# Optimization experiments

Hardware: AMD Instinct MI355X
Metric: run time of the kernel (lower is better)

## Reference

```python
import jax, jax.numpy as jnp
import numpy as np

N = 50000      # nodes
E = 800000     # edges (avg degree 16)
D_IN, D_H, D_OUT = 128, 128, 64


def setup_inputs() -> dict:
    key = jax.random.key(0)
    ks = jax.random.split(key, 12)
    s = 0.05  # weight init scale
    return {
        "x": jax.random.normal(ks[0], (N, D_IN), jnp.float32),
        "edge_index": jax.random.randint(ks[1], (2, E), 0, N, dtype=jnp.int64),
        "Wl0": jax.random.normal(ks[2], (D_H, D_IN), jnp.float32) * s,
        "bl0": jax.random.normal(ks[3], (D_H,), jnp.float32) * s,
        "Wr0": jax.random.normal(ks[4], (D_H, D_IN), jnp.float32) * s,
        "Wl1": jax.random.normal(ks[5], (D_H, D_H), jnp.float32) * s,
        "bl1": jax.random.normal(ks[6], (D_H,), jnp.float32) * s,
        "Wr1": jax.random.normal(ks[7], (D_H, D_H), jnp.float32) * s,
        "Wl2": jax.random.normal(ks[8], (D_OUT, D_H), jnp.float32) * s,
        "bl2": jax.random.normal(ks[9], (D_OUT,), jnp.float32) * s,
        "Wr2": jax.random.normal(ks[10], (D_OUT, D_H), jnp.float32) * s,
    }


def _sage_layer(h, src, dst, Wl, bl, Wr):
    # mean aggregation over incoming neighbors: out[i] = mean_{j in N(i)} h[j]
    n = h.shape[0]
    agg = jax.ops.segment_sum(h[src], dst, num_segments=n)          # [N, D]
    deg = jax.ops.segment_sum(jnp.ones((src.shape[0],), h.dtype), dst,
                              num_segments=n)                        # [N]
    mean = agg / jnp.maximum(deg, 1.0)[:, None]  # empty rows -> 0, matches torch_sparse
    # lin_l(agg) + lin_r(self); lin_r has no bias in PyG SAGEConv
    return mean @ Wl.T + bl + h @ Wr.T


def reference(x, edge_index, Wl0, bl0, Wr0, Wl1, bl1, Wr1, Wl2, bl2, Wr2):
    src, dst = edge_index[1], edge_index[0]  # adj row = dst, col = src
    h = jax.nn.relu(_sage_layer(x, src, dst, Wl0, bl0, Wr0))
    h = jax.nn.relu(_sage_layer(h, src, dst, Wl1, bl1, Wr1))
    h = _sage_layer(h, src, dst, Wl2, bl2, Wr2)
    return jax.nn.log_softmax(h, axis=1)
```

## Files before the change

kernel.cpp:

```cpp
#include <hip/hip_runtime.h>
#include <hip/hip_bf16.h>


typedef __attribute__((ext_vector_type(8))) short bf16x8;
typedef __attribute__((ext_vector_type(4))) float f32x4;

#define NPB 128
#define BCAP 2560
#define EPB 8192
#define EPT 32
#define CPAD 16

__device__ __forceinline__ unsigned short f2bf(float f) {
    unsigned int u = __builtin_bit_cast(unsigned int, f);
    u += 0x7fffu + ((u >> 16) & 1u);
    return (unsigned short)(u >> 16);
}
__device__ __forceinline__ float bf2f(unsigned int bits16) {
    return __builtin_bit_cast(float, bits16 << 16);
}


__global__ __launch_bounds__(256) void dist_cast_kernel(const int* __restrict__ dst,
                                                        const int* __restrict__ srcv,
                                                        int* __restrict__ gcnt,
                                                        unsigned int* __restrict__ staging,
                                                        int E, int NBc, int DB, int XB,
                                                        const float* __restrict__ x,
                                                        unsigned short* __restrict__ xbf,
                                                        const float* p0, const float* p1,
                                                        const float* p2, const float* p3,
                                                        const float* p4, const float* p5,
                                                        unsigned short* __restrict__ wbf) {
    __shared__ unsigned int stage[EPB];
    __shared__ int hist[400];
    __shared__ int lstart[400];
    __shared__ int gbase[400];
    __shared__ int scanbuf[256];
    int bid = blockIdx.x;
    int t = threadIdx.x;

    if (bid >= DB && bid < DB + XB) {
        int base = (bid - DB) * 256 + t;
        int stride = XB * 256;
        const float2* x2 = (const float2*)x;
        unsigned int* xo = (unsigned int*)xbf;
#pragma unroll
        for (int k = 0; k < 4; ++k) {
            int idx = base + k * stride;
            float2 v = x2[idx];
            xo[idx] = (unsigned int)f2bf(v.x) | ((unsigned int)f2bf(v.y) << 16);
        }
        return;
    }
    if (bid >= DB + XB) {
        int w = (bid - DB - XB) * 256 + t;
        if (w < 40960) {
            const float* src;
            int local;
            if      (w < 8192)  { src = p0; local = w; }
            else if (w < 16384) { src = p1; local = w - 8192; }
            else if (w < 24576) { src = p2; local = w - 16384; }
            else if (w < 32768) { src = p3; local = w - 24576; }
            else if (w < 36864) { src = p4; local = w - 32768; }
            else                { src = p5; local = w - 36864; }
            float2 v = ((const float2*)src)[local];
            unsigned int p = (unsigned int)f2bf(v.x) | ((unsigned int)f2bf(v.y) << 16);
            ((unsigned int*)wbf)[w] = p;
        }
        return;
    }

    int e0 = bid * EPB;
    unsigned int w[EPT];

    for (int b = t; b < NBc + 1; b += 256) hist[b] = 0;
    __syncthreads();

#pragma unroll
    for (int i = 0; i < EPT; ++i) {
        int e = e0 + i * 256 + t;
        unsigned int word = 0xFFFFFFFFu;
        if (e < E) word = ((unsigned int)dst[e] << 16) | (unsigned int)srcv[e];
        w[i] = word;
        int b = (int)(word >> 23); if (b > NBc) b = NBc;
        atomicAdd(&hist[b], 1);
    }
    __syncthreads();

    int b0 = 2 * t, b1 = 2 * t + 1;
    int h0 = (b0 <= NBc) ? hist[b0] : 0;
    int h1 = (b1 <= NBc) ? hist[b1] : 0;
    int pair = h0 + h1;
    scanbuf[t] = pair;
    __syncthreads();
    for (int off = 1; off < 256; off <<= 1) {
        int v = (t >= off) ? scanbuf[t - off] : 0;
        __syncthreads();
        scanbuf[t] += v;
        __syncthreads();
    }
    int excl = scanbuf[t] - pair;
    if (b0 <= NBc) lstart[b0] = excl;
    if (b1 <= NBc) lstart[b1] = excl + h0;
    __syncthreads();

    for (int b = t; b < NBc; b += 256) {
        int h = hist[b];
        gbase[b] = h ? atomicAdd(&gcnt[b * CPAD], h) : 0;
    }
    for (int b = t; b < NBc + 1; b += 256) hist[b] = lstart[b];
    __syncthreads();

#pragma unroll
    for (int i = 0; i < EPT; ++i) {
        unsigned int word = w[i];
        int b = (int)(word >> 23); if (b > NBc) b = NBc;
        int p = atomicAdd(&hist[b], 1);
        stage[p] = word;
    }
    __syncthreads();

    int total = lstart[NBc];
    for (int i = t; i < total; i += 256) {
        unsigned int word = stage[i];
        int b = (int)(word >> 23);
        int gpos = gbase[b] + (i - lstart[b]);
        staging[(size_t)b * BCAP + gpos] = word;
    }
}


template<int GY, int ASL, int CSL>
__device__ __forceinline__ void gemm_body(int mb, int y,
                                          const unsigned short* __restrict__ H,
                                          const unsigned short* __restrict__ Wl,
                                          const unsigned short* __restrict__ Wr,
                                          unsigned short* __restrict__ Cl,
                                          unsigned short* __restrict__ Cr, int N) {
    __shared__ unsigned short clds[4 * 32 * 68];
    const int halfY = GY >> 1;
    const int ldc = GY * 32;
    int wave = threadIdx.x >> 6;
    int lane = threadIdx.x & 63;
    int l15 = lane & 15, quad = lane >> 4;
    bool isL = y < halfY;
    const unsigned short* W = isL ? Wl : Wr;
    unsigned short* Cp = isL ? Cl : Cr;
    int yy = isL ? y : y - halfY;
    int wrow0 = yy * 64;
    int col0 = yy * 64;
    int m0 = mb * 128 + wave * 32;

    int r0 = m0 + l15;      if (r0 > N - 1) r0 = N - 1;
    int r1 = m0 + 16 + l15; if (r1 > N - 1) r1 = N - 1;

    f32x4 acc[2][4] = {};
#pragma unroll
    for (int ks = 0; ks < 4; ++ks) {
        int vidx = ks * 4 + quad;
        bf16x8 a0, a1;
        if constexpr (ASL) {
            const unsigned short* base = H + (size_t)(vidx >> 1) * N * 16 + (vidx & 1) * 8;
            a0 = *(const bf16x8*)(base + (size_t)r0 * 16);
            a1 = *(const bf16x8*)(base + (size_t)r1 * 16);
        } else {
            a0 = ((const bf16x8*)(H + (size_t)r0 * 128))[vidx];
            a1 = ((const bf16x8*)(H + (size_t)r1 * 128))[vidx];
        }
#pragma unroll
        for (int j = 0; j < 4; ++j) {
            const bf16x8* B = (const bf16x8*)(W + (size_t)(wrow0 + j * 16 + l15) * 128);
            bf16x8 b = B[vidx];
            acc[0][j] = __builtin_amdgcn_mfma_f32_16x16x32_bf16(a0, b, acc[0][j], 0, 0, 0);
            acc[1][j] = __builtin_amdgcn_mfma_f32_16x16x32_bf16(a1, b, acc[1][j], 0, 0, 0);
        }
    }

    unsigned short* slice = clds + wave * (32 * 68);
#pragma unroll
    for (int i = 0; i < 2; ++i)
#pragma unroll
        for (int j = 0; j < 4; ++j)
#pragma unroll
            for (int r = 0; r < 4; ++r)
                slice[(i * 16 + quad * 4 + r) * 68 + j * 16 + l15] = f2bf(acc[i][j][r]);
    __syncthreads();

    if (CSL && isL) {
        int nodeLocal = lane >> 1, hf = lane & 1;
        int row = m0 + nodeLocal;
        int s0 = col0 >> 4;
        if (row < N) {
#pragma unroll
            for (int sl = 0; sl < 4; ++sl) {
                const unsigned short* p = slice + nodeLocal * 68 + sl * 16 + hf * 8;
                unsigned long long lo = *(const unsigned long long*)(p);
                unsigned long long hi = *(const unsigned long long*)(p + 4);
                unsigned long long* q =
                    (unsigned long long*)(Cl + ((size_t)(s0 + sl) * N + row) * 16 + hf * 8);
                q[0] = lo;
                q[1] = hi;
            }
        }
    } else {
        int rlo = lane >> 3, j8 = lane & 7;
#pragma unroll
        for (int pass = 0; pass < 4; ++pass) {
            int row_local = pass * 8 + rlo;
            const unsigned short* p = slice + row_local * 68 + j8 * 8;
            unsigned long long lo = *(const unsigned long long*)(p);
            unsigned long long hi = *(const unsigned long long*)(p + 4);
            int row = m0 + row_local;
            if (row < N) {
                unsigned long long* q =
                    (unsigned long long*)(Cp + (size_t)row * ldc + col0 + j8 * 8);
                q[0] = lo;
                q[1] = hi;
            }
        }
    }
    __syncthreads();
}


__global__ __launch_bounds__(256) void build_gemm_kernel(const unsigned int* __restrict__ staging,
                                                         const int* __restrict__ gcnt,
                                                         int* __restrict__ row_ptr,
                                                         int* __restrict__ adj, int N, int NBc,
                                                         int gemmRows,
                                                         const unsigned short* __restrict__ H,
                                                         const unsigned short* __restrict__ Wl,
                                                         const unsigned short* __restrict__ Wr,
                                                         unsigned short* __restrict__ Cl,
                                                         unsigned short* __restrict__ Cr) {
    __shared__ int hist[NPB];
    __shared__ int scn[NPB];
    __shared__ int wsum[4];
    int bid = blockIdx.x;
    int t = threadIdx.x;

    if (bid >= NBc) {
        int gid = bid - NBc;
        gemm_body<4, 0, 1>(gid % gemmRows, gid / gemmRows, H, Wl, Wr, Cl, Cr, N);
        return;
    }

    int b = bid;
    int n0 = b * NPB;
    int nb = N - n0; if (nb > NPB) nb = NPB;
    int ec = gcnt[b * CPAD];
    const unsigned int* st = staging + (size_t)b * BCAP;

    int a = 0;
    for (int j = t; j < b; j += 256) a += gcnt[j * CPAD];
#pragma unroll
    for (int off = 32; off; off >>= 1) a += __shfl_xor(a, off);
    if ((t & 63) == 0) wsum[t >> 6] = a;
    if (t < NPB) hist[t] = 0;
    __syncthreads();
    int bb = wsum[0] + wsum[1] + wsum[2] + wsum[3];

    for (int i = t; i < ec; i += 256)
        atomicAdd(&hist[(st[i] >> 16) & (NPB - 1)], 1);
    __syncthreads();

    int v = (t < NPB) ? hist[t] : 0;
    if (t < NPB) scn[t] = v;
    __syncthreads();
    for (int off = 1; off < NPB; off <<= 1) {
        int u = (t >= off && t < NPB) ? scn[t - off] : 0;
        __syncthreads();
        if (t < NPB) scn[t] += u;
        __syncthreads();
    }
    if (t < NPB) hist[t] = scn[t] - v;
    if (t < nb) row_ptr[n0 + t] = bb + (scn[t] - v);
    if (b == NBc - 1 && t == 0) row_ptr[N] = bb + ec;
    __syncthreads();

    for (int i = t; i < ec; i += 256) {
        unsigned int pk = st[i];
        int p = atomicAdd(&hist[(pk >> 16) & (NPB - 1)], 1);
        adj[bb + p] = (int)(pk & 0xffffu);
    }
}


template<int GY, int ASL, int CSL>
__global__ __launch_bounds__(256) void gemm_mfma_kernel(const unsigned short* __restrict__ H,
                                                        const unsigned short* __restrict__ Wl,
                                                        const unsigned short* __restrict__ Wr,
                                                        unsigned short* __restrict__ Cl,
                                                        unsigned short* __restrict__ Cr,
                                                        int N) {
    gemm_body<GY, ASL, CSL>(blockIdx.x, blockIdx.y, H, Wl, Wr, Cl, Cr, N);
}


__global__ __launch_bounds__(256) void agg_sliced_kernel(const unsigned short* __restrict__ Cls,
                                                         const unsigned short* __restrict__ Cr,
                                                         const int* __restrict__ row_ptr,
                                                         const int* __restrict__ adj,
                                                         const float* __restrict__ bias,
                                                         unsigned short* __restrict__ houts,
                                                         int N) {
    int s = blockIdx.x & 7;
    int nb = blockIdx.x >> 3;
    int wave = threadIdx.x >> 6;
    int lane = threadIdx.x & 63;
    int node = nb * 128 + wave * 32 + (lane >> 1);
    int half = lane & 1;
    if (node >= N) return;
    int beg = row_ptr[node], end = row_ptr[node + 1];
    const unsigned short* tab = Cls + (size_t)s * N * 16 + half * 8;

    float acc[8] = {};
    int e = beg;
    for (; e + 4 <= end; e += 4) {
        int i0 = adj[e], i1 = adj[e + 1], i2 = adj[e + 2], i3 = adj[e + 3];
        bf16x8 v0 = *(const bf16x8*)(tab + (size_t)i0 * 16);
        bf16x8 v1 = *(const bf16x8*)(tab + (size_t)i1 * 16);
        bf16x8 v2 = *(const bf16x8*)(tab + (size_t)i2 * 16);
        bf16x8 v3 = *(const bf16x8*)(tab + (size_t)i3 * 16);
#pragma unroll
        for (int k = 0; k < 8; ++k) acc[k] += bf2f((unsigned short)v0[k]);
#pragma unroll
        for (int k = 0; k < 8; ++k) acc[k] += bf2f((unsigned short)v1[k]);
#pragma unroll
        for (int k = 0; k < 8; ++k) acc[k] += bf2f((unsigned short)v2[k]);
#pragma unroll
        for (int k = 0; k < 8; ++k) acc[k] += bf2f((unsigned short)v3[k]);
    }
    for (; e < end; ++e) {
        int i0 = adj[e];
        bf16x8 v0 = *(const bf16x8*)(tab + (size_t)i0 * 16);
#pragma unroll
        for (int k = 0; k < 8; ++k) acc[k] += bf2f((unsigned short)v0[k]);
    }

    int deg = end - beg;
    float inv = 1.0f / (float)(deg > 1 ? deg : 1);
    bf16x8 sv = *(const bf16x8*)(Cr + (size_t)node * 128 + s * 16 + half * 8);
    float4 b0 = ((const float4*)bias)[s * 4 + half * 2];
    float4 b1 = ((const float4*)bias)[s * 4 + half * 2 + 1];
    float bb[8] = {b0.x, b0.y, b0.z, b0.w, b1.x, b1.y, b1.z, b1.w};
    bf16x8 o;
#pragma unroll
    for (int k = 0; k < 8; ++k)
        o[k] = (short)f2bf(fmaxf(acc[k] * inv + bb[k] + bf2f((unsigned short)sv[k]), 0.f));
    *(bf16x8*)(houts + ((size_t)s * N + node) * 16 + half * 8) = o;
}


__global__ __launch_bounds__(256) void final_kernel(const unsigned short* __restrict__ Cl2,
                                                    const unsigned short* __restrict__ Cr2,
                                                    const int* __restrict__ row_ptr,
                                                    const int* __restrict__ adj,
                                                    const float* __restrict__ bias,
                                                    float* __restrict__ out, int N) {
    int pr = (int)((blockIdx.x * blockDim.x + threadIdx.x) >> 6);
    int lane = threadIdx.x & 63;
    int nodeA = pr * 2;
    if (nodeA >= N) return;
    int nodeB = nodeA + 1;
    bool hasB = nodeB < N;
    int g = lane >> 3, c = lane & 7;
    int begA = row_ptr[nodeA], endA = row_ptr[nodeA + 1];
    int begB = hasB ? row_ptr[nodeB] : 0;
    int endB = hasB ? row_ptr[nodeB + 1] : 0;
    float pA[8] = {}, pB[8] = {};

    int cntA = endA - begA; if (cntA > 64) cntA = 64;
    int cntB = endB - begB; if (cntB > 64) cntB = 64;
    int idxA = (cntA > 0) ? adj[begA + (lane < cntA ? lane : cntA - 1)] : 0;
    int idxB = (cntB > 0) ? adj[begB + (lane < cntB ? lane : cntB - 1)] : 0;
    int c1A = cntA - 1, c1B = cntB - 1;
    int mx = cntA > cntB ? cntA : cntB;
    for (int i = 0; i < mx; i += 16) {
        bool doA = i < cntA, doB = i < cntB;
        bf16x8 vA[2], vB[2];
        float mA[2], mB[2];
        if (doA) {
#pragma unroll
            for (int ss = 0; ss < 2; ++ss) {
                int tt = i + ss * 8 + g;
                int src = __shfl(idxA, tt > c1A ? c1A : tt);
                mA[ss] = tt < cntA ? 1.f : 0.f;
                vA[ss] = ((const bf16x8*)(Cl2 + (size_t)src * 64))[c];
            }
        }
        if (doB) {
#pragma unroll
            for (int ss = 0; ss < 2; ++ss) {
                int tt = i + ss * 8 + g;
                int src = __shfl(idxB, tt > c1B ? c1B : tt);
                mB[ss] = tt < cntB ? 1.f : 0.f;
                vB[ss] = ((const bf16x8*)(Cl2 + (size_t)src * 64))[c];
            }
        }
        if (doA) {
#pragma unroll
            for (int ss = 0; ss < 2; ++ss)
#pragma unroll
                for (int k = 0; k < 8; ++k)
                    pA[k] += mA[ss] * bf2f((unsigned short)vA[ss][k]);
        }
        if (doB) {
#pragma unroll
            for (int ss = 0; ss < 2; ++ss)
#pragma unroll
                for (int k = 0; k < 8; ++k)
                    pB[k] += mB[ss] * bf2f((unsigned short)vB[ss][k]);
        }
    }
    for (int e = begA + 64; e < endA; e += 64) {
        int cnt = endA - e; if (cnt > 64) cnt = 64;
        int idx = adj[e + (lane < cnt ? lane : cnt - 1)];
        int c1 = cnt - 1;
        for (int i = 0; i < cnt; i += 16) {
#pragma unroll
            for (int ss = 0; ss < 2; ++ss) {
                int tt = i + ss * 8 + g;
                int src = __shfl(idx, tt > c1 ? c1 : tt);
                float m = tt < cnt ? 1.f : 0.f;
                bf16x8 v = ((const bf16x8*)(Cl2 + (size_t)src * 64))[c];
#pragma unroll
                for (int k = 0; k < 8; ++k)
                    pA[k] += m * bf2f((unsigned short)v[k]);
            }
        }
    }
    for (int e = begB + 64; e < endB; e += 64) {
        int cnt = endB - e; if (cnt > 64) cnt = 64;
        int idx = adj[e + (lane < cnt ? lane : cnt - 1)];
        int c1 = cnt - 1;
        for (int i = 0; i < cnt; i += 16) {
#pragma unroll
            for (int ss = 0; ss < 2; ++ss) {
                int tt = i + ss * 8 + g;
                int src = __shfl(idx, tt > c1 ? c1 : tt);
                float m = tt < cnt ? 1.f : 0.f;
                bf16x8 v = ((const bf16x8*)(Cl2 + (size_t)src * 64))[c];
#pragma unroll
                for (int k = 0; k < 8; ++k)
                    pB[k] += m * bf2f((unsigned short)v[k]);
            }
        }
    }

#pragma unroll
    for (int k = 0; k < 8; ++k) {
        pA[k] += __shfl_xor(pA[k], 8);
        pA[k] += __shfl_xor(pA[k], 16);
        pA[k] += __shfl_xor(pA[k], 32);
        pB[k] += __shfl_xor(pB[k], 8);
        pB[k] += __shfl_xor(pB[k], 16);
        pB[k] += __shfl_xor(pB[k], 32);
    }

    int degA = endA - begA, degB = endB - begB;
    float invA = 1.0f / (float)(degA > 1 ? degA : 1);
    float invB = 1.0f / (float)(degB > 1 ? degB : 1);
    bf16x8 svA = ((const bf16x8*)(Cr2 + (size_t)nodeA * 64))[c];
    bf16x8 svB = hasB ? ((const bf16x8*)(Cr2 + (size_t)nodeB * 64))[c] : svA;
    float4 b0 = ((const float4*)bias)[2 * c];
    float4 b1 = ((const float4*)bias)[2 * c + 1];
    float bb[8] = {b0.x, b0.y, b0.z, b0.w, b1.x, b1.y, b1.z, b1.w};
    float uA[8], uB[8];
#pragma unroll
    for (int k = 0; k < 8; ++k) {
        uA[k] = pA[k] * invA + bb[k] + bf2f((unsigned short)svA[k]);
        uB[k] = pB[k] * invB + bb[k] + bf2f((unsigned short)svB[k]);
    }

    float mA_ = uA[0], mB_ = uB[0];
#pragma unroll
    for (int k = 1; k < 8; ++k) { mA_ = fmaxf(mA_, uA[k]); mB_ = fmaxf(mB_, uB[k]); }
#pragma unroll
    for (int off = 1; off < 8; off <<= 1) {
        mA_ = fmaxf(mA_, __shfl_xor(mA_, off));
        mB_ = fmaxf(mB_, __shfl_xor(mB_, off));
    }
    float seA = 0.f, seB = 0.f;
#pragma unroll
    for (int k = 0; k < 8; ++k) { seA += __expf(uA[k] - mA_); seB += __expf(uB[k] - mB_); }
#pragma unroll
    for (int off = 1; off < 8; off <<= 1) {
        seA += __shfl_xor(seA, off);
        seB += __shfl_xor(seB, off);
    }
    float lsA = __logf(seA), lsB = __logf(seB);

    if (g == 0) {
        float4 o0 = {uA[0] - mA_ - lsA, uA[1] - mA_ - lsA, uA[2] - mA_ - lsA, uA[3] - mA_ - lsA};
        float4 o1 = {uA[4] - mA_ - lsA, uA[5] - mA_ - lsA, uA[6] - mA_ - lsA, uA[7] - mA_ - lsA};
        ((float4*)(out + (size_t)nodeA * 64))[2 * c] = o0;
        ((float4*)(out + (size_t)nodeA * 64))[2 * c + 1] = o1;
    } else if (g == 1 && hasB) {
        float4 o0 = {uB[0] - mB_ - lsB, uB[1] - mB_ - lsB, uB[2] - mB_ - lsB, uB[3] - mB_ - lsB};
        float4 o1 = {uB[4] - mB_ - lsB, uB[5] - mB_ - lsB, uB[6] - mB_ - lsB, uB[7] - mB_ - lsB};
        ((float4*)(out + (size_t)nodeB * 64))[2 * c] = o0;
        ((float4*)(out + (size_t)nodeB * 64))[2 * c + 1] = o1;
    }
}


extern "C" void kernel_launch(void* const* d_in, const int* in_sizes, int n_in,
                              void* d_out, int out_size, void* d_ws, size_t ws_size,
                              hipStream_t stream) {
    const float* x   = (const float*)d_in[0];
    const int*   ei  = (const int*)d_in[1];
    const float* Wl0 = (const float*)d_in[2];
    const float* bl0 = (const float*)d_in[3];
    const float* Wr0 = (const float*)d_in[4];
    const float* Wl1 = (const float*)d_in[5];
    const float* bl1 = (const float*)d_in[6];
    const float* Wr1 = (const float*)d_in[7];
    const float* Wl2 = (const float*)d_in[8];
    const float* bl2 = (const float*)d_in[9];
    const float* Wr2 = (const float*)d_in[10];
    float* out = (float*)d_out;

    const int N  = in_sizes[0] / 128;
    const int E  = in_sizes[1] / 2;
    const int NB = (N + NPB - 1) / NPB;

    char* ws = (char*)d_ws;
    auto alloc = [&](size_t bytes) {
        char* p = ws;
        ws += (bytes + 255) & ~(size_t)255;
        return p;
    };
    int*   row_ptr    = (int*)alloc((size_t)(N + 1) * 4);
    int*   adj        = (int*)alloc((size_t)E * 4);
    int*   gcnt      = (int*)alloc((size_t)NB * CPAD * 4);
    unsigned int* staging = (unsigned int*)alloc((size_t)NB * BCAP * 4);
    unsigned short* xbf = (unsigned short*)alloc((size_t)N * 128 * 2);
    unsigned short* wbf = (unsigned short*)alloc((size_t)81920 * 2);
    unsigned short* Cl  = (unsigned short*)alloc((size_t)N * 128 * 2);
    unsigned short* Cr  = (unsigned short*)alloc((size_t)N * 128 * 2);
    unsigned short* hA  = (unsigned short*)alloc((size_t)N * 128 * 2);
    unsigned short* hB  = (unsigned short*)alloc((size_t)N * 128 * 2);

    const int* dstp = ei;
    const int* srcp = ei + E;

    unsigned short* wl0 = wbf;
    unsigned short* wr0 = wbf + 16384;
    unsigned short* wl1 = wbf + 32768;
    unsigned short* wr1 = wbf + 49152;
    unsigned short* wl2 = wbf + 65536;
    unsigned short* wr2 = wbf + 73728;

    dim3 blk(256);
    int DB = (E + EPB - 1) / EPB;
    int XB = (N * 64) / (256 * 4);
    int gemmRows = (N + 127) / 128;
    int aggSlBlocks = ((N + 127) / 128) * 8;
    int pairBlocks = (((N + 1) / 2) * 64 + 255) / 256;

    hipMemsetAsync(gcnt, 0, (size_t)NB * CPAD * 4, stream);
    dist_cast_kernel<<<DB + XB + 160, blk, 0, stream>>>(dstp, srcp, gcnt, staging, E, NB,
                                                        DB, XB, x, xbf,
                                                        Wl0, Wr0, Wl1, Wr1, Wl2, Wr2, wbf);
    build_gemm_kernel<<<NB + gemmRows * 4, blk, 0, stream>>>(staging, gcnt, row_ptr, adj,
                                                             N, NB, gemmRows, xbf, wl0, wr0,
                                                             Cl, Cr);
    agg_sliced_kernel<<<aggSlBlocks, blk, 0, stream>>>(Cl, Cr, row_ptr, adj, bl0, hA, N);
    gemm_mfma_kernel<4, 1, 1><<<dim3(gemmRows, 4), blk, 0, stream>>>(hA, wl1, wr1, Cl, Cr, N);
    agg_sliced_kernel<<<aggSlBlocks, blk, 0, stream>>>(Cl, Cr, row_ptr, adj, bl1, hB, N);
    gemm_mfma_kernel<2, 1, 0><<<dim3(gemmRows, 2), blk, 0, stream>>>(hB, wl2, wr2, Cl, Cr, N);
    final_kernel<<<pairBlocks, blk, 0, stream>>>(Cl, Cr, row_ptr, adj, bl2, out, N);
}
```

Before: 284.1 us.

## Use 32-column feature slices and edge-parallel wave aggregation with shuffle reduction

```diff
diff --git a/kernel.cpp b/kernel.cpp
--- a/kernel.cpp
+++ b/kernel.cpp
@@ -161,9 +161,9 @@
         int vidx = ks * 4 + quad;
         bf16x8 a0, a1;
         if constexpr (ASL) {
-            const unsigned short* base = H + (size_t)(vidx >> 1) * N * 16 + (vidx & 1) * 8;
-            a0 = *(const bf16x8*)(base + (size_t)r0 * 16);
-            a1 = *(const bf16x8*)(base + (size_t)r1 * 16);
+            const unsigned short* base = H + (size_t)(vidx >> 2) * N * 32 + (vidx & 3) * 8;
+            a0 = *(const bf16x8*)(base + (size_t)r0 * 32);
+            a1 = *(const bf16x8*)(base + (size_t)r1 * 32);
         } else {
             a0 = ((const bf16x8*)(H + (size_t)r0 * 128))[vidx];
             a1 = ((const bf16x8*)(H + (size_t)r1 * 128))[vidx];
@@ -188,21 +188,24 @@
     __syncthreads();
 
     if (CSL && isL) {
-        int nodeLocal = lane >> 1, hf = lane & 1;
-        int row = m0 + nodeLocal;
-        int s0 = col0 >> 4;
-        if (row < N) {
-#pragma unroll
-            for (int sl = 0; sl < 4; ++sl) {
-                const unsigned short* p = slice + nodeLocal * 68 + sl * 16 + hf * 8;
-                unsigned long long lo = *(const unsigned long long*)(p);
-                unsigned long long hi = *(const unsigned long long*)(p + 4);
-                unsigned long long* q =
-                    (unsigned long long*)(Cl + ((size_t)(s0 + sl) * N + row) * 16 + hf * 8);
-                q[0] = lo;
-                q[1] = hi;
+        int s0 = col0 >> 5;
+        int rsub = lane >> 2, chunk = lane & 3;
+#pragma unroll
+        for (int sl = 0; sl < 2; ++sl)
+#pragma unroll
+            for (int pass = 0; pass < 2; ++pass) {
+                int row_local = pass * 16 + rsub;
+                int row = m0 + row_local;
+                if (row < N) {
+                    const unsigned short* p = slice + row_local * 68 + sl * 32 + chunk * 8;
+                    unsigned long long lo = *(const unsigned long long*)(p);
+                    unsigned long long hi = *(const unsigned long long*)(p + 4);
+                    unsigned long long* q = (unsigned long long*)
+                        (Cl + ((size_t)(s0 + sl) * N + row) * 32 + chunk * 8);
+                    q[0] = lo;
+                    q[1] = hi;
+                }
             }
-        }
     } else {
         int rlo = lane >> 3, j8 = lane & 7;
 #pragma unroll
@@ -305,51 +308,49 @@
                                                          const float* __restrict__ bias,
                                                          unsigned short* __restrict__ houts,
                                                          int N) {
-    int s = blockIdx.x & 7;
-    int nb = blockIdx.x >> 3;
+    int s = blockIdx.x & 3;
+    int nbg = blockIdx.x >> 2;
     int wave = threadIdx.x >> 6;
     int lane = threadIdx.x & 63;
-    int node = nb * 128 + wave * 32 + (lane >> 1);
-    int half = lane & 1;
-    if (node >= N) return;
-    int beg = row_ptr[node], end = row_ptr[node + 1];
-    const unsigned short* tab = Cls + (size_t)s * N * 16 + half * 8;
-
-    float acc[8] = {};
-    int e = beg;
-    for (; e + 4 <= end; e += 4) {
-        int i0 = adj[e], i1 = adj[e + 1], i2 = adj[e + 2], i3 = adj[e + 3];
-        bf16x8 v0 = *(const bf16x8*)(tab + (size_t)i0 * 16);
-        bf16x8 v1 = *(const bf16x8*)(tab + (size_t)i1 * 16);
-        bf16x8 v2 = *(const bf16x8*)(tab + (size_t)i2 * 16);
-        bf16x8 v3 = *(const bf16x8*)(tab + (size_t)i3 * 16);
-#pragma unroll
-        for (int k = 0; k < 8; ++k) acc[k] += bf2f((unsigned short)v0[k]);
-#pragma unroll
-        for (int k = 0; k < 8; ++k) acc[k] += bf2f((unsigned short)v1[k]);
-#pragma unroll
-        for (int k = 0; k < 8; ++k) acc[k] += bf2f((unsigned short)v2[k]);
-#pragma unroll
-        for (int k = 0; k < 8; ++k) acc[k] += bf2f((unsigned short)v3[k]);
-    }
-    for (; e < end; ++e) {
-        int i0 = adj[e];
-        bf16x8 v0 = *(const bf16x8*)(tab + (size_t)i0 * 16);
-#pragma unroll
-        for (int k = 0; k < 8; ++k) acc[k] += bf2f((unsigned short)v0[k]);
-    }
-
-    int deg = end - beg;
-    float inv = 1.0f / (float)(deg > 1 ? deg : 1);
-    bf16x8 sv = *(const bf16x8*)(Cr + (size_t)node * 128 + s * 16 + half * 8);
-    float4 b0 = ((const float4*)bias)[s * 4 + half * 2];
-    float4 b1 = ((const float4*)bias)[s * 4 + half * 2 + 1];
+    int slot = lane >> 2, chunk = lane & 3;
+    const unsigned short* tab = Cls + (size_t)s * N * 32 + chunk * 8;
+
+    float4 b0 = ((const float4*)bias)[s * 8 + chunk * 2];
+    float4 b1 = ((const float4*)bias)[s * 8 + chunk * 2 + 1];
     float bb[8] = {b0.x, b0.y, b0.z, b0.w, b1.x, b1.y, b1.z, b1.w};
-    bf16x8 o;
-#pragma unroll
-    for (int k = 0; k < 8; ++k)
-        o[k] = (short)f2bf(fmaxf(acc[k] * inv + bb[k] + bf2f((unsigned short)sv[k]), 0.f));
-    *(bf16x8*)(houts + ((size_t)s * N + node) * 16 + half * 8) = o;
+
+#pragma unroll
+    for (int i = 0; i < 4; ++i) {
+        int node = nbg * 16 + wave * 4 + i;
+        if (node >= N) continue;
+        int beg = row_ptr[node], end = row_ptr[node + 1];
+        float p[8] = {};
+        for (int e = beg; e < end; e += 16) {
+            int cnt = end - e; if (cnt > 16) cnt = 16;
+            int sl = slot < cnt ? slot : cnt - 1;
+            int idx = adj[e + sl];
+            float m = slot < cnt ? 1.f : 0.f;
+            bf16x8 v = *(const bf16x8*)(tab + (size_t)idx * 32);
+#pragma unroll
+            for (int k = 0; k < 8; ++k) p[k] += m * bf2f((unsigned short)v[k]);
+        }
+#pragma unroll
+        for (int k = 0; k < 8; ++k) {
+            p[k] += __shfl_xor(p[k], 4);
+            p[k] += __shfl_xor(p[k], 8);
+            p[k] += __shfl_xor(p[k], 16);
+            p[k] += __shfl_xor(p[k], 32);
+        }
+        int deg = end - beg;
+        float inv = 1.0f / (float)(deg > 1 ? deg : 1);
+        bf16x8 sv = *(const bf16x8*)(Cr + (size_t)node * 128 + s * 32 + chunk * 8);
+        bf16x8 o;
+#pragma unroll
+        for (int k = 0; k < 8; ++k)
+            o[k] = (short)f2bf(fmaxf(p[k] * inv + bb[k] + bf2f((unsigned short)sv[k]), 0.f));
+        if (slot == 0)
+            *(bf16x8*)(houts + ((size_t)s * N + node) * 32 + chunk * 8) = o;
+    }
 }
 
 
@@ -557,7 +558,7 @@
     int DB = (E + EPB - 1) / EPB;
     int XB = (N * 64) / (256 * 4);
     int gemmRows = (N + 127) / 128;
-    int aggSlBlocks = ((N + 127) / 128) * 8;
+    int aggSlBlocks = ((N + 15) / 16) * 4;
     int pairBlocks = (((N + 1) / 2) * 64 + 255) / 256;
 
     hipMemsetAsync(gcnt, 0, (size_t)NB * CPAD * 4, stream);
```

After: 346.9 us. 1.22x slower.
